# Kernel tuning notes

Hardware: AMD Instinct MI355X
Metric: run time of the kernel (lower is better)

Reference implementation:

```python
import jax, jax.numpy as jnp
import numpy as np

SIGMA_NEU = 0.05
SIGMA_SYN = 0.002
JIJ_STD = 0.045


def setup_inputs() -> dict:
    key = jax.random.key(0)
    ks = jax.random.split(key, 6)
    B, T, n_in, n_hid, n_out = 64, 64, 128, 256, 32
    input_signal = jax.random.normal(ks[0], (B, T, n_in), dtype=jnp.float32)
    hidden = jax.random.normal(ks[1], (B, n_hid), dtype=jnp.float32)
    # nn.Linear default init approximated by scaled normals; w_hh uses uniform(-jij_std, jij_std)
    w_in_w = jax.random.normal(ks[2], (n_hid, n_in), dtype=jnp.float32) / np.sqrt(n_in)
    w_hh_w = jax.random.uniform(ks[3], (n_hid, n_hid), minval=-JIJ_STD, maxval=JIJ_STD, dtype=jnp.float32)
    w_hh_b = jnp.zeros((n_hid,), dtype=jnp.float32)
    w_out_w = jax.random.normal(ks[4], (n_out, n_hid), dtype=jnp.float32) / np.sqrt(n_hid)
    alpha = jnp.full((n_hid,), 0.25, dtype=jnp.float32)
    beta = jnp.full((n_hid,), 0.1, dtype=jnp.float32)
    return {
        "input_signal": input_signal,
        "hidden": hidden,
        "length": T,
        "w_in_w": w_in_w,
        "w_hh_w": w_hh_w,
        "w_hh_b": w_hh_b,
        "w_out_w": w_out_w,
        "alpha": alpha,
        "beta": beta,
    }


def reference(input_signal, hidden, length, w_in_w, w_hh_w, w_hh_b, w_out_w, alpha, beta):
    # tanh activation, beta != 0 branch, anti-Hebbian plasticity.
    B, T, n_in = input_signal.shape
    n_hid = hidden.shape[1]
    x = jnp.transpose(input_signal, (1, 0, 2))  # (T, B, n_in)
    keys = jax.random.split(jax.random.key(42), length)
    sqrt_alpha = jnp.sqrt(alpha)
    sqrt_beta = jnp.sqrt(beta)
    # Track only different_j = new_j - w_hh (starts at 0); new_j never needed separately.
    diff_j0 = jnp.zeros((B, n_hid, n_hid), dtype=input_signal.dtype)

    def step(carry, inp):
        h, diff_j = carry
        xt, k = inp
        k1, k2 = jax.random.split(k)
        act = jnp.tanh(h)
        # row-vector times per-sample fast-weight matrix: (b,1,n) @ (b,n,n) -> (b,n)
        dj_act = jnp.einsum('bi,bij->bj', act, diff_j)
        tmp = xt @ w_in_w.T + act @ w_hh_w.T + w_hh_b + dj_act
        neural_noise = jax.random.normal(k1, h.shape, h.dtype) * SIGMA_NEU * sqrt_alpha
        h = (1.0 - alpha) * h + alpha * tmp + neural_noise
        # anti-Hebbian: -outer(act, act) + syn noise (sqrt(beta) broadcasts on last dim)
        add_w = -jnp.einsum('bi,bj->bij', act, act) \
                + jax.random.normal(k2, diff_j.shape, diff_j.dtype) * SIGMA_SYN * sqrt_beta
        diff_j = diff_j + beta * add_w
        out = 20.0 * jnp.tanh(h @ w_out_w.T)
        return (h, diff_j), (h, out)

    (hidden, _), (h_seq, o_seq) = jax.lax.scan(step, (hidden, diff_j0), (x, keys))
    hidden_list = jnp.transpose(h_seq, (1, 0, 2))  # (B, T, n_hid)
    output_list = jnp.transpose(o_seq, (1, 0, 2))  # (B, T, n_out)
    return hidden_list, output_list, hidden
```

## Files before the change

### kernel.cpp

```cpp
#include <hip/hip_runtime.h>
#include <stdint.h>

#define BB 64
#define TT 64
#define NIN 128
#define NHID 256
#define NOUT 32
#define BPS 8
#define NBLK (BB * BPS)
#define NTHR 1024
#define JS 32

#define SIG_NEU 0.05f
#define SIG_SYN 0.002f

#define FLAG_OFF    0
#define FLAG_STRIDE 32
#define FLAG_BYTES  (BB * BPS * FLAG_STRIDE * 4)
#define HPUB_OFF    FLAG_BYTES

#define HID_LIST_SZ ((size_t)BB * TT * NHID)
#define OUT_LIST_SZ ((size_t)BB * TT * NOUT)

__device__ __forceinline__ uint32_t rotl32(uint32_t v, int s) {
  return (v << s) | (v >> (32 - s));
}

__device__ __forceinline__ void tf2x32(uint32_t k0, uint32_t k1, uint32_t x0, uint32_t x1,
                                       uint32_t& o0, uint32_t& o1) {
  const uint32_t k2 = k0 ^ k1 ^ 0x1BD11BDAu;
  x0 += k0; x1 += k1;
  x0 += x1; x1 = rotl32(x1,13); x1 ^= x0;
  x0 += x1; x1 = rotl32(x1,15); x1 ^= x0;
  x0 += x1; x1 = rotl32(x1,26); x1 ^= x0;
  x0 += x1; x1 = rotl32(x1, 6); x1 ^= x0;
  x0 += k1; x1 += k2 + 1u;
  x0 += x1; x1 = rotl32(x1,17); x1 ^= x0;
  x0 += x1; x1 = rotl32(x1,29); x1 ^= x0;
  x0 += x1; x1 = rotl32(x1,16); x1 ^= x0;
  x0 += x1; x1 = rotl32(x1,24); x1 ^= x0;
  x0 += k2; x1 += k0 + 2u;
  x0 += x1; x1 = rotl32(x1,13); x1 ^= x0;
  x0 += x1; x1 = rotl32(x1,15); x1 ^= x0;
  x0 += x1; x1 = rotl32(x1,26); x1 ^= x0;
  x0 += x1; x1 = rotl32(x1, 6); x1 ^= x0;
  x0 += k0; x1 += k1 + 3u;
  x0 += x1; x1 = rotl32(x1,17); x1 ^= x0;
  x0 += x1; x1 = rotl32(x1,29); x1 ^= x0;
  x0 += x1; x1 = rotl32(x1,16); x1 ^= x0;
  x0 += x1; x1 = rotl32(x1,24); x1 ^= x0;
  x0 += k1; x1 += k2 + 4u;
  x0 += x1; x1 = rotl32(x1,13); x1 ^= x0;
  x0 += x1; x1 = rotl32(x1,15); x1 ^= x0;
  x0 += x1; x1 = rotl32(x1,26); x1 ^= x0;
  x0 += x1; x1 = rotl32(x1, 6); x1 ^= x0;
  x0 += k2; x1 += k0 + 5u;
  o0 = x0; o1 = x1;
}

__device__ __forceinline__ float tf_normal(uint32_t k0, uint32_t k1, uint32_t idx) {
  uint32_t o0, o1;
  tf2x32(k0, k1, 0u, idx, o0, o1);
  const uint32_t bits = o0 ^ o1;
  const float u = __uint_as_float((bits >> 9) | 0x3f800000u) - 1.0f;
  float x = fmaf(u, 2.0f, -0.99999994f);
  x = fmaxf(x, -0.99999994f);
  const float w = -__logf(fmaf(-x, x, 1.0f));
  float p;
  if (w < 5.0f) {
    const float q = w - 2.5f;
    p = 2.81022636e-08f;
    p = fmaf(p, q, 3.43273939e-07f);
    p = fmaf(p, q, -3.5233877e-06f);
    p = fmaf(p, q, -4.39150654e-06f);
    p = fmaf(p, q, 0.00021858087f);
    p = fmaf(p, q, -0.00125372503f);
    p = fmaf(p, q, -0.00417768164f);
    p = fmaf(p, q, 0.246640727f);
    p = fmaf(p, q, 1.50140941f);
  } else {
    const float q = sqrtf(w) - 3.0f;
    p = -0.000200214257f;
    p = fmaf(p, q, 0.000100950558f);
    p = fmaf(p, q, 0.00134934322f);
    p = fmaf(p, q, -0.00367342844f);
    p = fmaf(p, q, 0.00573950773f);
    p = fmaf(p, q, -0.0076224613f);
    p = fmaf(p, q, 0.00943887047f);
    p = fmaf(p, q, 1.00167406f);
    p = fmaf(p, q, 2.83297682f);
  }
  return 1.41421356f * (p * x);
}

#define SPIN(slice, want)                                                         \
  do {                                                                            \
    uint32_t* fp_ = &flags[((b) * BPS + (slice)) * FLAG_STRIDE];                  \
    for (int it_ = 0; it_ < 300000; ++it_) {                                      \
      if (__hip_atomic_load(fp_, __ATOMIC_RELAXED, __HIP_MEMORY_SCOPE_AGENT) >=   \
          (uint32_t)(want)) break;                                                \
      __builtin_amdgcn_s_sleep(2);                                                \
    }                                                                             \
  } while (0)

__global__ __launch_bounds__(NTHR, 8) void rnn_kernel(
    const float* __restrict__ xin, const float* __restrict__ h0,
    const float* __restrict__ w_in, const float* __restrict__ w_hh,
    const float* __restrict__ b_hh, const float* __restrict__ w_out,
    const float* __restrict__ alpha, const float* __restrict__ beta,
    float* __restrict__ out, char* __restrict__ ws)
{
  __shared__ __align__(16) float wos[4 * 260];
  __shared__ __align__(16) float h_s[NHID];
  __shared__ __align__(16) float a_s[NHID];
  __shared__ __align__(16) float xt_s[NIN];
  __shared__ float stat_s[JS];
  __shared__ float djact_s[JS];
  __shared__ uint32_t keys_s[TT * 4];

  const int tid = threadIdx.x;
  const int blk = blockIdx.x;
  const int b   = blk & 63;
  const int s   = blk >> 6;

  uint32_t* flags = (uint32_t*)(ws + FLAG_OFF);
  float*    hpub  = (float*)(ws + HPUB_OFF);

  if (tid < TT) {
    uint32_t ka, kb, t0, t1;
    tf2x32(0u, 42u, 0u, (uint32_t)tid, ka, kb);
    tf2x32(ka, kb, 0u, 0u, t0, t1);
    keys_s[tid * 4 + 0] = t0; keys_s[tid * 4 + 1] = t1;
    tf2x32(ka, kb, 0u, 1u, t0, t1);
    keys_s[tid * 4 + 2] = t0; keys_s[tid * 4 + 3] = t1;
  }
  if (tid < NHID) {
    const float hv = h0[b * NHID + tid];
    h_s[tid] = hv;
    a_s[tid] = tanhf(hv);
  }
  {
    const int r = tid >> 8, c = tid & 255;
    wos[r * 260 + c] = w_out[(s * 4 + r) * NHID + c];
  }

  const int u  = tid & 31;
  const int c5 = tid >> 5;
  const int jg = s * JS + c5;
  const float bj  = beta[jg];
  const float sbj = SIG_SYN * sqrtf(bj);
  const uint32_t idxb = ((uint32_t)b << 16) | ((uint32_t)u << 8) | (uint32_t)jg;

  const float4 whr0 = *(const float4*)(w_hh + (size_t)jg * NHID + 0 * 128 + u * 4);
  const float4 whr1 = *(const float4*)(w_hh + (size_t)jg * NHID + 1 * 128 + u * 4);
  const float4 winr = *(const float4*)(w_in + (size_t)jg * NIN + u * 4);
  const float bias  = b_hh[jg];

  float r_al = 0.f, r_om = 0.f, r_ns = 0.f;
  uint32_t hnidx = 0;
  if (tid < JS) {
    r_al = alpha[s * JS + tid];
    r_om = 1.0f - r_al;
    r_ns = SIG_NEU * sqrtf(r_al);
    hnidx = (uint32_t)(b * NHID + s * JS + tid);
  }

  float d[8];
  #pragma unroll
  for (int r = 0; r < 8; ++r) d[r] = 0.0f;
  float n[8];
  float hn = 0.0f;

  __syncthreads();

  {
    const uint32_t k2a = __builtin_amdgcn_readfirstlane(keys_s[2]);
    const uint32_t k2b = __builtin_amdgcn_readfirstlane(keys_s[3]);
    #pragma unroll
    for (int r = 0; r < 8; ++r)
      n[r] = tf_normal(k2a, k2b, idxb + ((uint32_t)r << 13));
    if (tid < JS) {
      const uint32_t k1a = __builtin_amdgcn_readfirstlane(keys_s[0]);
      const uint32_t k1b = __builtin_amdgcn_readfirstlane(keys_s[1]);
      hn = tf_normal(k1a, k1b, hnidx);
    }
    if (tid < NIN) xt_s[tid] = xin[((size_t)b * TT) * NIN + tid];
  }
  __syncthreads();

  const int wv = tid >> 6;
  const int ln = tid & 63;

  for (int t = 0; t < TT; ++t) {
    const int par = t & 1;

    const float aj = a_s[jg];
    float pd = 0.0f;
    #pragma unroll
    for (int r = 0; r < 8; ++r) {
      const float ai = a_s[u + 32 * r];
      pd = fmaf(ai, d[r], pd);
      d[r] = fmaf(bj, fmaf(n[r], sbj, -ai * aj), d[r]);
    }
    pd += __shfl_xor(pd, 1);
    pd += __shfl_xor(pd, 2);
    pd += __shfl_xor(pd, 4);
    pd += __shfl_xor(pd, 8);
    pd += __shfl_xor(pd, 16);
    if (u == 0) djact_s[c5] = pd;

    {
      float acc = 0.0f;
      const float4 x4 = *((const float4*)xt_s + u);
      acc = fmaf(winr.x, x4.x, acc); acc = fmaf(winr.y, x4.y, acc);
      acc = fmaf(winr.z, x4.z, acc); acc = fmaf(winr.w, x4.w, acc);
      const float4 a0 = *((const float4*)a_s + u);
      acc = fmaf(whr0.x, a0.x, acc); acc = fmaf(whr0.y, a0.y, acc);
      acc = fmaf(whr0.z, a0.z, acc); acc = fmaf(whr0.w, a0.w, acc);
      const float4 a1 = *((const float4*)a_s + 32 + u);
      acc = fmaf(whr1.x, a1.x, acc); acc = fmaf(whr1.y, a1.y, acc);
      acc = fmaf(whr1.z, a1.z, acc); acc = fmaf(whr1.w, a1.w, acc);
      acc += __shfl_xor(acc, 1);
      acc += __shfl_xor(acc, 2);
      acc += __shfl_xor(acc, 4);
      acc += __shfl_xor(acc, 8);
      acc += __shfl_xor(acc, 16);
      if (u == 0) stat_s[c5] = acc + bias;
    }

    if (wv == 8 && t > 0) {
      const int o = ln >> 4, sub = ln & 15;
      float acc = 0.0f;
      #pragma unroll
      for (int q = 0; q < 4; ++q) {
        const float4 wvv = *(const float4*)(wos + o * 260 + q * 64 + sub * 4);
        const float4 hv  = *(const float4*)(h_s + q * 64 + sub * 4);
        acc = fmaf(wvv.x, hv.x, acc); acc = fmaf(wvv.y, hv.y, acc);
        acc = fmaf(wvv.z, hv.z, acc); acc = fmaf(wvv.w, hv.w, acc);
      }
      acc += __shfl_xor(acc, 8);
      acc += __shfl_xor(acc, 4);
      acc += __shfl_xor(acc, 2);
      acc += __shfl_xor(acc, 1);
      if (sub == 0)
        out[HID_LIST_SZ + ((size_t)b * TT + (t - 1)) * NOUT + s * 4 + o] =
            20.0f * tanhf(acc);
    }
    __syncthreads();

    if (tid < JS) {
      const float tmp  = stat_s[tid] + djact_s[tid];
      const float hnew = fmaf(r_al, tmp, r_om * h_s[s * JS + tid]) + hn * r_ns;
      __hip_atomic_store(&hpub[(par * BB + b) * NHID + s * JS + tid], hnew,
                         __ATOMIC_RELAXED, __HIP_MEMORY_SCOPE_AGENT);
    }
    if (tid == 0) {
      asm volatile("s_waitcnt vmcnt(0)" ::: "memory");
      __hip_atomic_store(&flags[(b * BPS + s) * FLAG_STRIDE], (uint32_t)(t + 1),
                         __ATOMIC_RELAXED, __HIP_MEMORY_SCOPE_AGENT);
    }
    if (t + 1 < TT) {
      const uint32_t k2a = __builtin_amdgcn_readfirstlane(keys_s[(t + 1) * 4 + 2]);
      const uint32_t k2b = __builtin_amdgcn_readfirstlane(keys_s[(t + 1) * 4 + 3]);
      #pragma unroll
      for (int r = 0; r < 8; ++r)
        n[r] = tf_normal(k2a, k2b, idxb + ((uint32_t)r << 13));
      if (tid < JS) {
        const uint32_t k1a = __builtin_amdgcn_readfirstlane(keys_s[(t + 1) * 4 + 0]);
        const uint32_t k1b = __builtin_amdgcn_readfirstlane(keys_s[(t + 1) * 4 + 1]);
        hn = tf_normal(k1a, k1b, hnidx);
      }
    }

    if (wv < 8) {
      if (ln == 0) SPIN(wv, t + 1);
      asm volatile("" ::: "memory");
      if (ln < JS) {
        const float hv = __hip_atomic_load(&hpub[(par * BB + b) * NHID + wv * JS + ln],
                                           __ATOMIC_RELAXED, __HIP_MEMORY_SCOPE_AGENT);
        h_s[wv * JS + ln] = hv;
        a_s[wv * JS + ln] = tanhf(hv);
      }
    } else if (wv < 12) {
      if (s == 0) {
        const int k = (wv - 8) * 64 + ln;
        if (ln == 0)       SPIN(2 * (wv - 8), t + 1);
        else if (ln == 32) SPIN(2 * (wv - 8) + 1, t + 1);
        asm volatile("" ::: "memory");
        const float hv = __hip_atomic_load(&hpub[(par * BB + b) * NHID + k],
                                           __ATOMIC_RELAXED, __HIP_MEMORY_SCOPE_AGENT);
        out[((size_t)b * TT + t) * NHID + k] = hv;
        if (t == TT - 1)
          out[HID_LIST_SZ + OUT_LIST_SZ + (size_t)b * NHID + k] = hv;
      }
    } else if (wv < 14) {
      const int k = (wv - 12) * 64 + ln;
      if (t + 1 < TT) xt_s[k] = xin[((size_t)b * TT + t + 1) * NIN + k];
    }
    __syncthreads();
  }

  if (wv == 8) {
    const int o = ln >> 4, sub = ln & 15;
    float acc = 0.0f;
    #pragma unroll
    for (int q = 0; q < 4; ++q) {
      const float4 wvv = *(const float4*)(wos + o * 260 + q * 64 + sub * 4);
      const float4 hv  = *(const float4*)(h_s + q * 64 + sub * 4);
      acc = fmaf(wvv.x, hv.x, acc); acc = fmaf(wvv.y, hv.y, acc);
      acc = fmaf(wvv.z, hv.z, acc); acc = fmaf(wvv.w, hv.w, acc);
    }
    acc += __shfl_xor(acc, 8);
    acc += __shfl_xor(acc, 4);
    acc += __shfl_xor(acc, 2);
    acc += __shfl_xor(acc, 1);
    if (sub == 0)
      out[HID_LIST_SZ + ((size_t)b * TT + (TT - 1)) * NOUT + s * 4 + o] =
          20.0f * tanhf(acc);
  }
}

extern "C" void kernel_launch(void* const* d_in, const int* in_sizes, int n_in,
                              void* d_out, int out_size, void* d_ws, size_t ws_size,
                              hipStream_t stream) {
  (void)in_sizes; (void)n_in; (void)out_size; (void)ws_size;
  const float* x     = (const float*)d_in[0];
  const float* h0    = (const float*)d_in[1];
  const float* w_in  = (const float*)d_in[3];
  const float* w_hh  = (const float*)d_in[4];
  const float* b_hh  = (const float*)d_in[5];
  const float* w_out = (const float*)d_in[6];
  const float* alpha = (const float*)d_in[7];
  const float* beta  = (const float*)d_in[8];
  float* out = (float*)d_out;

  hipMemsetAsync((char*)d_ws + FLAG_OFF, 0, FLAG_BYTES, stream);
  rnn_kernel<<<dim3(NBLK), dim3(NTHR), 0, stream>>>(
      x, h0, w_in, w_hh, b_hh, w_out, alpha, beta, out, (char*)d_ws);
}
```

Baseline: 1.008 ms.

## Halve blocks per sample and give each block 64 hidden units

Each batch sample is now split across 4 cooperating blocks instead of 8, so every block owns 64 hidden units with 16 lanes per row rather than 32. Each thread keeps 16 fast-weight entries and noise values in registers, and the output projection and h-publish/spin work are remapped to fit. Fewer blocks per sample means fewer cross-block flag waits and global h exchanges per timestep. In exchange each thread does twice the per-step fast-weight work and noise generation and uses more registers. The spin loop also sleeps for a shorter interval.

Result: slower. 1.157 ms (+14.8%).

```diff
diff --git a/kernel.cpp b/kernel.cpp
--- a/kernel.cpp
+++ b/kernel.cpp
@@ -6,10 +6,10 @@
 #define NIN 128
 #define NHID 256
 #define NOUT 32
-#define BPS 8
+#define BPS 4
 #define NBLK (BB * BPS)
 #define NTHR 1024
-#define JS 32
+#define JS 64
 
 #define SIG_NEU 0.05f
 #define SIG_SYN 0.002f
@@ -96,21 +96,21 @@
 #define SPIN(slice, want)                                                         \
   do {                                                                            \
     uint32_t* fp_ = &flags[((b) * BPS + (slice)) * FLAG_STRIDE];                  \
-    for (int it_ = 0; it_ < 300000; ++it_) {                                      \
+    for (int it_ = 0; it_ < 1000000; ++it_) {                                     \
       if (__hip_atomic_load(fp_, __ATOMIC_RELAXED, __HIP_MEMORY_SCOPE_AGENT) >=   \
           (uint32_t)(want)) break;                                                \
-      __builtin_amdgcn_s_sleep(2);                                                \
+      __builtin_amdgcn_s_sleep(1);                                                \
     }                                                                             \
   } while (0)
 
-__global__ __launch_bounds__(NTHR, 8) void rnn_kernel(
+__global__ __launch_bounds__(NTHR, 4) void rnn_kernel(
     const float* __restrict__ xin, const float* __restrict__ h0,
     const float* __restrict__ w_in, const float* __restrict__ w_hh,
     const float* __restrict__ b_hh, const float* __restrict__ w_out,
     const float* __restrict__ alpha, const float* __restrict__ beta,
     float* __restrict__ out, char* __restrict__ ws)
 {
-  __shared__ __align__(16) float wos[4 * 260];
+  __shared__ __align__(16) float wos[8 * 260];
   __shared__ __align__(16) float h_s[NHID];
   __shared__ __align__(16) float a_s[NHID];
   __shared__ __align__(16) float xt_s[NIN];
@@ -139,22 +139,28 @@
     h_s[tid] = hv;
     a_s[tid] = tanhf(hv);
   }
-  {
-    const int r = tid >> 8, c = tid & 255;
-    wos[r * 260 + c] = w_out[(s * 4 + r) * NHID + c];
-  }
-
-  const int u  = tid & 31;
-  const int c5 = tid >> 5;
-  const int jg = s * JS + c5;
+  #pragma unroll
+  for (int e = 0; e < 2; ++e) {
+    const int idx = tid + e * NTHR;
+    const int r = idx >> 8, c = idx & 255;
+    wos[r * 260 + c] = w_out[(s * 8 + r) * NHID + c];
+  }
+
+  const int q  = tid & 15;
+  const int jl = tid >> 4;
+  const int jg = s * JS + jl;
   const float bj  = beta[jg];
   const float sbj = SIG_SYN * sqrtf(bj);
-  const uint32_t idxb = ((uint32_t)b << 16) | ((uint32_t)u << 8) | (uint32_t)jg;
-
-  const float4 whr0 = *(const float4*)(w_hh + (size_t)jg * NHID + 0 * 128 + u * 4);
-  const float4 whr1 = *(const float4*)(w_hh + (size_t)jg * NHID + 1 * 128 + u * 4);
-  const float4 winr = *(const float4*)(w_in + (size_t)jg * NIN + u * 4);
-  const float bias  = b_hh[jg];
+  const uint32_t idxb = ((uint32_t)b << 16) | ((uint32_t)q << 8) | (uint32_t)jg;
+
+  float4 whr[4], winr[2];
+  #pragma unroll
+  for (int k = 0; k < 4; ++k)
+    whr[k] = *(const float4*)(w_hh + (size_t)jg * NHID + q * 16 + k * 4);
+  #pragma unroll
+  for (int k = 0; k < 2; ++k)
+    winr[k] = *(const float4*)(w_in + (size_t)jg * NIN + q * 8 + k * 4);
+  const float bias = b_hh[jg];
 
   float r_al = 0.f, r_om = 0.f, r_ns = 0.f;
   uint32_t hnidx = 0;
@@ -165,10 +171,10 @@
     hnidx = (uint32_t)(b * NHID + s * JS + tid);
   }
 
-  float d[8];
+  float d[16];
   #pragma unroll
-  for (int r = 0; r < 8; ++r) d[r] = 0.0f;
-  float n[8];
+  for (int r = 0; r < 16; ++r) d[r] = 0.0f;
+  float n[16];
   float hn = 0.0f;
 
   __syncthreads();
@@ -177,8 +183,8 @@
     const uint32_t k2a = __builtin_amdgcn_readfirstlane(keys_s[2]);
     const uint32_t k2b = __builtin_amdgcn_readfirstlane(keys_s[3]);
     #pragma unroll
-    for (int r = 0; r < 8; ++r)
-      n[r] = tf_normal(k2a, k2b, idxb + ((uint32_t)r << 13));
+    for (int r = 0; r < 16; ++r)
+      n[r] = tf_normal(k2a, k2b, idxb + ((uint32_t)r << 12));
     if (tid < JS) {
       const uint32_t k1a = __builtin_amdgcn_readfirstlane(keys_s[0]);
       const uint32_t k1b = __builtin_amdgcn_readfirstlane(keys_s[1]);
@@ -197,8 +203,8 @@
     const float aj = a_s[jg];
     float pd = 0.0f;
     #pragma unroll
-    for (int r = 0; r < 8; ++r) {
-      const float ai = a_s[u + 32 * r];
+    for (int r = 0; r < 16; ++r) {
+      const float ai = a_s[q + 16 * r];
       pd = fmaf(ai, d[r], pd);
       d[r] = fmaf(bj, fmaf(n[r], sbj, -ai * aj), d[r]);
     }
@@ -206,44 +212,44 @@
     pd += __shfl_xor(pd, 2);
     pd += __shfl_xor(pd, 4);
     pd += __shfl_xor(pd, 8);
-    pd += __shfl_xor(pd, 16);
-    if (u == 0) djact_s[c5] = pd;
+    if (q == 0) djact_s[jl] = pd;
 
     {
       float acc = 0.0f;
-      const float4 x4 = *((const float4*)xt_s + u);
-      acc = fmaf(winr.x, x4.x, acc); acc = fmaf(winr.y, x4.y, acc);
-      acc = fmaf(winr.z, x4.z, acc); acc = fmaf(winr.w, x4.w, acc);
-      const float4 a0 = *((const float4*)a_s + u);
-      acc = fmaf(whr0.x, a0.x, acc); acc = fmaf(whr0.y, a0.y, acc);
-      acc = fmaf(whr0.z, a0.z, acc); acc = fmaf(whr0.w, a0.w, acc);
-      const float4 a1 = *((const float4*)a_s + 32 + u);
-      acc = fmaf(whr1.x, a1.x, acc); acc = fmaf(whr1.y, a1.y, acc);
-      acc = fmaf(whr1.z, a1.z, acc); acc = fmaf(whr1.w, a1.w, acc);
+      #pragma unroll
+      for (int k = 0; k < 2; ++k) {
+        const float4 xv = *(const float4*)(xt_s + q * 8 + k * 4);
+        acc = fmaf(winr[k].x, xv.x, acc); acc = fmaf(winr[k].y, xv.y, acc);
+        acc = fmaf(winr[k].z, xv.z, acc); acc = fmaf(winr[k].w, xv.w, acc);
+      }
+      #pragma unroll
+      for (int k = 0; k < 4; ++k) {
+        const float4 av = *(const float4*)(a_s + q * 16 + k * 4);
+        acc = fmaf(whr[k].x, av.x, acc); acc = fmaf(whr[k].y, av.y, acc);
+        acc = fmaf(whr[k].z, av.z, acc); acc = fmaf(whr[k].w, av.w, acc);
+      }
       acc += __shfl_xor(acc, 1);
       acc += __shfl_xor(acc, 2);
       acc += __shfl_xor(acc, 4);
       acc += __shfl_xor(acc, 8);
-      acc += __shfl_xor(acc, 16);
-      if (u == 0) stat_s[c5] = acc + bias;
-    }
-
-    if (wv == 8 && t > 0) {
-      const int o = ln >> 4, sub = ln & 15;
+      if (q == 0) stat_s[jl] = acc + bias;
+    }
+
+    if (wv == 15 && t > 0) {
+      const int o = ln >> 3, sub = ln & 7;
       float acc = 0.0f;
       #pragma unroll
-      for (int q = 0; q < 4; ++q) {
-        const float4 wvv = *(const float4*)(wos + o * 260 + q * 64 + sub * 4);
-        const float4 hv  = *(const float4*)(h_s + q * 64 + sub * 4);
+      for (int k = 0; k < 8; ++k) {
+        const float4 wvv = *(const float4*)(wos + o * 260 + sub * 32 + k * 4);
+        const float4 hv  = *(const float4*)(h_s + sub * 32 + k * 4);
         acc = fmaf(wvv.x, hv.x, acc); acc = fmaf(wvv.y, hv.y, acc);
         acc = fmaf(wvv.z, hv.z, acc); acc = fmaf(wvv.w, hv.w, acc);
       }
-      acc += __shfl_xor(acc, 8);
+      acc += __shfl_xor(acc, 1);
+      acc += __shfl_xor(acc, 2);
       acc += __shfl_xor(acc, 4);
-      acc += __shfl_xor(acc, 2);
-      acc += __shfl_xor(acc, 1);
       if (sub == 0)
-        out[HID_LIST_SZ + ((size_t)b * TT + (t - 1)) * NOUT + s * 4 + o] =
+        out[HID_LIST_SZ + ((size_t)b * TT + (t - 1)) * NOUT + s * 8 + o] =
             20.0f * tanhf(acc);
     }
     __syncthreads();
@@ -263,8 +269,8 @@
       const uint32_t k2a = __builtin_amdgcn_readfirstlane(keys_s[(t + 1) * 4 + 2]);
       const uint32_t k2b = __builtin_amdgcn_readfirstlane(keys_s[(t + 1) * 4 + 3]);
       #pragma unroll
-      for (int r = 0; r < 8; ++r)
-        n[r] = tf_normal(k2a, k2b, idxb + ((uint32_t)r << 13));
+      for (int r = 0; r < 16; ++r)
+        n[r] = tf_normal(k2a, k2b, idxb + ((uint32_t)r << 12));
       if (tid < JS) {
         const uint32_t k1a = __builtin_amdgcn_readfirstlane(keys_s[(t + 1) * 4 + 0]);
         const uint32_t k1b = __builtin_amdgcn_readfirstlane(keys_s[(t + 1) * 4 + 1]);
@@ -272,20 +278,18 @@
       }
     }
 
-    if (wv < 8) {
+    if (wv < 4) {
       if (ln == 0) SPIN(wv, t + 1);
       asm volatile("" ::: "memory");
-      if (ln < JS) {
-        const float hv = __hip_atomic_load(&hpub[(par * BB + b) * NHID + wv * JS + ln],
-                                           __ATOMIC_RELAXED, __HIP_MEMORY_SCOPE_AGENT);
-        h_s[wv * JS + ln] = hv;
-        a_s[wv * JS + ln] = tanhf(hv);
-      }
-    } else if (wv < 12) {
+      const float hv = __hip_atomic_load(&hpub[(par * BB + b) * NHID + wv * JS + ln],
+                                         __ATOMIC_RELAXED, __HIP_MEMORY_SCOPE_AGENT);
+      h_s[wv * JS + ln] = hv;
+      a_s[wv * JS + ln] = tanhf(hv);
+    } else if (wv < 8) {
       if (s == 0) {
-        const int k = (wv - 8) * 64 + ln;
-        if (ln == 0)       SPIN(2 * (wv - 8), t + 1);
-        else if (ln == 32) SPIN(2 * (wv - 8) + 1, t + 1);
+        const int sl = wv - 4;
+        const int k  = sl * JS + ln;
+        if (ln == 0) SPIN(sl, t + 1);
         asm volatile("" ::: "memory");
         const float hv = __hip_atomic_load(&hpub[(par * BB + b) * NHID + k],
                                            __ATOMIC_RELAXED, __HIP_MEMORY_SCOPE_AGENT);
@@ -293,29 +297,28 @@
         if (t == TT - 1)
           out[HID_LIST_SZ + OUT_LIST_SZ + (size_t)b * NHID + k] = hv;
       }
-    } else if (wv < 14) {
-      const int k = (wv - 12) * 64 + ln;
+    } else if (wv < 10) {
+      const int k = (wv - 8) * 64 + ln;
       if (t + 1 < TT) xt_s[k] = xin[((size_t)b * TT + t + 1) * NIN + k];
     }
     __syncthreads();
   }
 
-  if (wv == 8) {
-    const int o = ln >> 4, sub = ln & 15;
+  if (wv == 15) {
+    const int o = ln >> 3, sub = ln & 7;
     float acc = 0.0f;
     #pragma unroll
-    for (int q = 0; q < 4; ++q) {
-      const float4 wvv = *(const float4*)(wos + o * 260 + q * 64 + sub * 4);
-      const float4 hv  = *(const float4*)(h_s + q * 64 + sub * 4);
+    for (int k = 0; k < 8; ++k) {
+      const float4 wvv = *(const float4*)(wos + o * 260 + sub * 32 + k * 4);
+      const float4 hv  = *(const float4*)(h_s + sub * 32 + k * 4);
       acc = fmaf(wvv.x, hv.x, acc); acc = fmaf(wvv.y, hv.y, acc);
       acc = fmaf(wvv.z, hv.z, acc); acc = fmaf(wvv.w, hv.w, acc);
     }
-    acc += __shfl_xor(acc, 8);
+    acc += __shfl_xor(acc, 1);
+    acc += __shfl_xor(acc, 2);
     acc += __shfl_xor(acc, 4);
-    acc += __shfl_xor(acc, 2);
-    acc += __shfl_xor(acc, 1);
     if (sub == 0)
-      out[HID_LIST_SZ + ((size_t)b * TT + (TT - 1)) * NOUT + s * 4 + o] =
+      out[HID_LIST_SZ + ((size_t)b * TT + (TT - 1)) * NOUT + s * 8 + o] =
           20.0f * tanhf(acc);
   }
 }
```
